# Kernel optimization log

Measured on AMD Instinct MI355X. Metric: run time of the kernel, lower is better.

Reference implementation:

```python
import jax, jax.numpy as jnp
import numpy as np

K_MASK = -2.3819763e+38
ROTARY_DIM = 80        # int(128 * 0.625), already even
ROPE_THETA = 1000000.0
NORM_EPS = 1e-6


def apply_rope(x, positions, head_dim, rope_theta):
    # x: [B, T, n, head_dim]; positions: [B, T]
    fraction = 2.0 * jnp.arange(0, head_dim // 2, dtype=jnp.float32) / head_dim
    timescale = rope_theta ** fraction                      # [hd/2]
    sinusoid = positions.astype(jnp.float32)[..., None] / timescale[None, None, :]
    sinusoid = sinusoid[..., None, :]                       # [B, T, 1, hd/2]
    sin = jnp.sin(sinusoid).astype(x.dtype)
    cos = jnp.cos(sinusoid).astype(x.dtype)
    first, second = jnp.split(x, 2, axis=-1)
    return jnp.concatenate(
        [first * cos - second * sin, second * cos + first * sin], axis=-1
    ).astype(x.dtype)


def rms_norm(x, w, eps=NORM_EPS):
    # Qwen3.5 convention: x/rms * (1 + w), w zero-initialized
    out = x * jax.lax.rsqrt(jnp.mean(x * x, axis=-1, keepdims=True) + eps)
    return out * (1.0 + w)


def setup_inputs() -> dict:
    B, T, D, N, K, H = 4, 1024, 4096, 32, 8, 128
    key = jax.random.key(0)
    ks = jax.random.split(key, 5)
    return {
        "x": jax.random.normal(ks[0], (B, T, D), jnp.float32),
        "positions": jnp.tile(jnp.arange(T, dtype=jnp.int32)[None, :], (B, 1)),
        "wq": jax.random.normal(ks[1], (D, N, 2 * H), jnp.float32) * 0.02,
        "wk": jax.random.normal(ks[2], (D, K, H), jnp.float32) * 0.02,
        "wv": jax.random.normal(ks[3], (D, K, H), jnp.float32) * 0.02,
        "wo": jax.random.normal(ks[4], (N, H, D), jnp.float32) * 0.02,
        "q_norm_w": jnp.zeros((H,), jnp.float32),
        "k_norm_w": jnp.zeros((H,), jnp.float32),
    }


def reference(x, positions, wq, wk, wv, wo, q_norm_w, k_norm_w):
    H = wk.shape[-1]
    # QKV projections; q_proj produces head_dim*2 -> (query, sigmoid gate)
    qg = jnp.einsum('BTD,DNH->BTNH', x, wq)            # [B,T,N,2H]
    q, gate = jnp.split(qg, 2, axis=-1)                # [B,T,N,H] each
    k = jnp.einsum('BSD,DKH->BSKH', x, wk)             # [B,S,K,H]
    v = jnp.einsum('BSD,DKH->BSKH', x, wv)             # [B,S,K,H]
    # per-head RMSNorm (Qwen3.5 style)
    q = rms_norm(q, q_norm_w)
    k = rms_norm(k, k_norm_w)
    # partial RoPE on first ROTARY_DIM dims of each head
    q = jnp.concatenate(
        [apply_rope(q[..., :ROTARY_DIM], positions, ROTARY_DIM, ROPE_THETA),
         q[..., ROTARY_DIM:]], axis=-1)
    k = jnp.concatenate(
        [apply_rope(k[..., :ROTARY_DIM], positions, ROTARY_DIM, ROPE_THETA),
         k[..., ROTARY_DIM:]], axis=-1)
    B, T, N, _ = q.shape
    Kh = k.shape[2]
    G = N // Kh                                        # GQA group size
    qg5 = q.reshape(B, T, Kh, G, H)
    scores = jnp.einsum('BTKGH,BSKH->BKGTS', qg5, k) * (H ** -0.5)
    causal = jnp.tril(jnp.ones((T, T), dtype=bool))    # [T,S]
    scores = jnp.where(causal[None, None, None, :, :], scores, K_MASK)
    probs = jax.nn.softmax(scores, axis=-1)
    out = jnp.einsum('BKGTS,BSKH->BTKGH', probs, v).reshape(B, T, N, H)
    out = out * jax.nn.sigmoid(gate)                   # gated attention output
    return jnp.einsum('BTNH,NHD->BTD', out, wo)
```

## Files before the change

### kernel.cpp

```cpp
#include <hip/hip_runtime.h>
#include <cstdint>
#include <cstddef>


typedef __attribute__((ext_vector_type(8))) short short8;
typedef __attribute__((ext_vector_type(4))) float float4v;

__device__ __forceinline__ unsigned short f2bf(float f) {
  unsigned u = __builtin_bit_cast(unsigned, f);
  u += 0x7fffu + ((u >> 16) & 1u);
  return (unsigned short)(u >> 16);
}
__device__ __forceinline__ float bf2f(unsigned short h) {
  unsigned u = ((unsigned)h) << 16;
  return __builtin_bit_cast(float, u);
}

__device__ __forceinline__ void gload_lds16(const void* g, void* l) {
  typedef const __attribute__((address_space(1))) void as1_cv;
  typedef __attribute__((address_space(3))) void as3_v;
  __builtin_amdgcn_global_load_lds((as1_cv*)g, (as3_v*)l, 16, 0, 0);
}

__global__ __launch_bounds__(256) void transpose_cvt(
    const float* __restrict__ src, unsigned short* __restrict__ dst,
    int R, int C) {
  __shared__ float tile[32][33];
  const int c0 = blockIdx.x * 32, r0 = blockIdx.y * 32;
  for (int i = threadIdx.y; i < 32; i += 8)
    tile[i][threadIdx.x] = src[(size_t)(r0 + i) * C + c0 + threadIdx.x];
  __syncthreads();
  for (int i = threadIdx.y; i < 32; i += 8)
    dst[(size_t)(c0 + i) * R + r0 + threadIdx.x] = f2bf(tile[threadIdx.x][i]);
}

__global__ __launch_bounds__(256) void cvt_f32_bf16(
    const float* __restrict__ src, unsigned short* __restrict__ dst, int n4) {
  int i = blockIdx.x * blockDim.x + threadIdx.x;
  if (i >= n4) return;
  float4 f = ((const float4*)src)[i];
  ushort4 o;
  o.x = f2bf(f.x); o.y = f2bf(f.y); o.z = f2bf(f.z); o.w = f2bf(f.w);
  ((ushort4*)dst)[i] = o;
}

__global__ __launch_bounds__(256) void v_transpose(
    const unsigned short* __restrict__ qkv, unsigned short* __restrict__ vtb) {
  __shared__ unsigned short tile[64][65];
  const int t0 = blockIdx.x * 64, h0 = blockIdx.y * 64;
  const int bk = blockIdx.z, b = bk >> 3, kh = bk & 7;
  const int tx = threadIdx.x & 63, ty = threadIdx.x >> 6;
  const unsigned short* src =
      qkv + (size_t)(b * 1024 + t0) * 10240 + 9216 + kh * 128 + h0;
  for (int i = ty; i < 64; i += 4)
    tile[i][tx] = src[(size_t)i * 10240 + tx];
  __syncthreads();
  unsigned short* dst = vtb + ((size_t)bk * 128 + h0) * 1024 + t0;
  for (int i = ty; i < 64; i += 4)
    dst[(size_t)i * 1024 + tx] = tile[tx][i];
}

template <bool BF16OUT>
__global__ __launch_bounds__(512, 2) void gemm_bt256(
    const unsigned short* __restrict__ A, const unsigned short* __restrict__ BT,
    void* __restrict__ Cv, int M, int N, int Kd) {
  __shared__ unsigned short As[4][256 * 32];
  __shared__ unsigned short Bs[4][256 * 32];

  const int tid = threadIdx.x;
  const int lane = tid & 63;
  const int wv = tid >> 6;
  const int wr = wv >> 2, wc = wv & 3;
  const int m0 = blockIdx.y * 256, n0 = blockIdx.x * 256;
  const int ml = lane & 15, q = lane >> 4;

  const int sr = tid >> 2;
  const int pc = tid & 3;
  const int gc = (pc ^ ((sr >> 1) & 3)) * 8;
  const unsigned short* gA0 = A + (size_t)(m0 + sr) * Kd + gc;
  const unsigned short* gB0 = BT + (size_t)(n0 + sr) * Kd + gc;
  const unsigned short* gA1 = gA0 + (size_t)128 * Kd;
  const unsigned short* gB1 = gB0 + (size_t)128 * Kd;
  const int lo0 = tid * 8;
  const int lo1 = 4096 + tid * 8;

  const int rdc = (q ^ ((ml >> 1) & 3)) * 8;
  const int aOff = (wr * 128 + ml) * 32 + rdc;
  const int bOff = (wc * 64 + ml) * 32 + rdc;

  float4v acc[8][4];
#pragma unroll
  for (int i = 0; i < 8; ++i)
#pragma unroll
    for (int j = 0; j < 4; ++j) acc[i][j] = (float4v)0.0f;

  const int NT = Kd >> 5;

#pragma unroll
  for (int t = 0; t < 3; ++t) {
    gload_lds16(gA0 + t * 32, &As[t][lo0]);
    gload_lds16(gA1 + t * 32, &As[t][lo1]);
    gload_lds16(gB0 + t * 32, &Bs[t][lo0]);
    gload_lds16(gB1 + t * 32, &Bs[t][lo1]);
  }
  asm volatile("s_waitcnt vmcnt(8)" ::: "memory");
  __builtin_amdgcn_s_barrier();

  for (int T = 0; T < NT; ++T) {
    const int buf = T & 3;
    const bool doStage = (T + 3 < NT);
    const int sb = (T + 3) & 3;
    const int gk = (T + 3) * 32;

    short8 bfr[4], af[4];
#pragma unroll
    for (int j = 0; j < 4; ++j)
      bfr[j] = *(const short8*)&Bs[buf][bOff + j * 512];
#pragma unroll
    for (int i = 0; i < 4; ++i)
      af[i] = *(const short8*)&As[buf][aOff + i * 512];
    if (doStage) {
      gload_lds16(gA0 + gk, &As[sb][lo0]);
      gload_lds16(gB0 + gk, &Bs[sb][lo0]);
    }
    __builtin_amdgcn_s_barrier();
    asm volatile("s_waitcnt lgkmcnt(0)" ::: "memory");
    __builtin_amdgcn_sched_barrier(0);
    __builtin_amdgcn_s_setprio(1);
#pragma unroll
    for (int i = 0; i < 4; ++i)
#pragma unroll
      for (int j = 0; j < 4; ++j)
        acc[i][j] = __builtin_amdgcn_mfma_f32_16x16x32_bf16(af[i], bfr[j], acc[i][j], 0, 0, 0);
    __builtin_amdgcn_s_setprio(0);
    __builtin_amdgcn_s_barrier();

#pragma unroll
    for (int i = 0; i < 4; ++i)
      af[i] = *(const short8*)&As[buf][aOff + 2048 + i * 512];
    if (doStage) {
      gload_lds16(gA1 + gk, &As[sb][lo1]);
      gload_lds16(gB1 + gk, &Bs[sb][lo1]);
    }
    __builtin_amdgcn_s_barrier();
    asm volatile("s_waitcnt lgkmcnt(0)" ::: "memory");
    __builtin_amdgcn_sched_barrier(0);
    __builtin_amdgcn_s_setprio(1);
#pragma unroll
    for (int i = 0; i < 4; ++i)
#pragma unroll
      for (int j = 0; j < 4; ++j)
        acc[4 + i][j] = __builtin_amdgcn_mfma_f32_16x16x32_bf16(af[i], bfr[j], acc[4 + i][j], 0, 0, 0);
    __builtin_amdgcn_s_setprio(0);
    if (T + 3 < NT)
      asm volatile("s_waitcnt vmcnt(8)" ::: "memory");
    else if (T + 2 < NT)
      asm volatile("s_waitcnt vmcnt(4)" ::: "memory");
    else if (T + 1 < NT)
      asm volatile("s_waitcnt vmcnt(0)" ::: "memory");
    __builtin_amdgcn_s_barrier();
  }

#pragma unroll
  for (int i = 0; i < 8; ++i) {
#pragma unroll
    for (int j = 0; j < 4; ++j) {
      const int grow = m0 + wr * 128 + i * 16 + q * 4;
      const int gcol = n0 + wc * 64 + j * 16 + ml;
#pragma unroll
      for (int r = 0; r < 4; ++r) {
        size_t idx = (size_t)(grow + r) * N + gcol;
        if constexpr (BF16OUT)
          ((unsigned short*)Cv)[idx] = f2bf(acc[i][j][r]);
        else
          ((float*)Cv)[idx] = acc[i][j][r];
      }
    }
  }
}

__global__ __launch_bounds__(256) void postproc_kernel(
    const unsigned short* __restrict__ qkv, const int* __restrict__ positions,
    const float* __restrict__ qnw, const float* __restrict__ knw,
    unsigned short* __restrict__ q_rot, unsigned short* __restrict__ sgb,
    unsigned short* __restrict__ k_rot) {
  const int wave = threadIdx.x >> 6, lane = threadIdx.x & 63;
  const int gslot = blockIdx.x * 4 + wave;
  const int m = gslot / 40, hs = gslot % 40;
  const int b = m >> 10, t = m & 1023;

  const unsigned short* base = (hs < 32)
      ? qkv + (size_t)m * 10240 + hs * 256
      : qkv + (size_t)m * 10240 + 8192 + (hs - 32) * 128;

  float v1 = bf2f(base[lane]);
  float v2 = bf2f(base[64 + lane]);

  float ss = v1 * v1 + v2 * v2;
  for (int off = 32; off > 0; off >>= 1) ss += __shfl_xor(ss, off);
  const float r = rsqrtf(ss * (1.0f / 128.0f) + 1e-6f);
  const float* nw = (hs < 32) ? qnw : knw;
  v1 *= r * (1.0f + nw[lane]);
  v2 *= r * (1.0f + nw[64 + lane]);

  const float pos = (float)positions[m];
  const int i1 = (lane < 40) ? lane : lane - 40;
  const float ang1 = pos * expf(-0.3453877639491068f * (float)i1);
  const float s1 = sinf(ang1), c1 = cosf(ang1);
  const float ang2 = pos * expf(-0.3453877639491068f * (float)(lane + 24));
  const float s2 = sinf(ang2), c2 = cosf(ang2);

  const float shA1 = __shfl(v1, (lane + 40) & 63);
  const float shA2 = __shfl(v2, (lane + 40) & 63);
  const float shX = __shfl(v1, (lane + 24) & 63);
  const float pA = (lane < 24) ? shA1 : shA2;
  const float o1 = (lane < 40) ? (v1 * c1 - pA * s1) : (v1 * c1 + shX * s1);
  const float o2 = (lane < 16) ? (v2 * c2 + shX * s2) : v2;

  if (hs < 32) {
    size_t qb = ((size_t)m * 32 + hs) * 128;
    q_rot[qb + lane] = f2bf(o1);
    q_rot[qb + 64 + lane] = f2bf(o2);
    float g1 = bf2f(base[128 + lane]), g2 = bf2f(base[192 + lane]);
    sgb[qb + lane] = f2bf(1.0f / (1.0f + expf(-g1)));
    sgb[qb + 64 + lane] = f2bf(1.0f / (1.0f + expf(-g2)));
  } else {
    const int kh = hs - 32;
    size_t kb = ((size_t)(b * 8 + kh) * 1024 + t) * 128;
    k_rot[kb + lane] = f2bf(o1);
    k_rot[kb + 64 + lane] = f2bf(o2);
  }
}

__global__ __launch_bounds__(256) void attn_kernel(
    const unsigned short* __restrict__ q_rot, const unsigned short* __restrict__ k_rot,
    const unsigned short* __restrict__ vt, const unsigned short* __restrict__ sgate,
    unsigned short* __restrict__ attn_out) {
  __shared__ unsigned short Ks[64 * 128];
  __shared__ unsigned short Vts[128 * 64];
  __shared__ unsigned short Ps[64 * 72];

  const int tid = threadIdx.x;
  const int lane = tid & 63, w = tid >> 6;
  const int qt = blockIdx.x & 15;
  const int n = (blockIdx.x >> 4) & 31;
  const int b = blockIdx.x >> 9;
  const int kh = n >> 2;
  const int t0 = qt * 64;
  const int ml = lane & 15, q = lane >> 4;
  const float SCALE = 0.08838834764831845f;

  short8 aq[4];
  {
    const unsigned short* qp =
        q_rot + (((size_t)(b * 1024 + t0 + w * 16 + ml)) * 32 + n) * 128 + q * 8;
#pragma unroll
    for (int ks = 0; ks < 4; ++ks) aq[ks] = *(const short8*)(qp + ks * 32);
  }

  float4v O[8];
#pragma unroll
  for (int i = 0; i < 8; ++i) O[i] = (float4v)0.0f;
  float mrow[4] = {-3e38f, -3e38f, -3e38f, -3e38f};
  float lrow[4] = {0.f, 0.f, 0.f, 0.f};

  const unsigned short* kbase = k_rot + (size_t)(b * 8 + kh) * 1024 * 128;
  const unsigned short* vbase = vt + (size_t)(b * 8 + kh) * 128 * 1024;
  const int rK = tid >> 4, cK = tid & 15;
  const int cKsw = (cK ^ rK) * 8;
  const int rV = tid >> 3, cV = tid & 7;
  const int cVsw = (cV ^ (rV & 7)) * 8;

  for (int si = 0; si <= qt; ++si) {
    const int s0 = si * 64;
#pragma unroll
    for (int it = 0; it < 4; ++it) {
      const int li = it * 256 + tid;
      gload_lds16(kbase + (size_t)(s0 + rK + it * 16) * 128 + cKsw, &Ks[li * 8]);
      gload_lds16(vbase + (size_t)(rV + it * 32) * 1024 + s0 + cVsw, &Vts[li * 8]);
    }
    __syncthreads();

    float4v Sv[4];
#pragma unroll
    for (int j = 0; j < 4; ++j) Sv[j] = (float4v)0.0f;
#pragma unroll
    for (int ks = 0; ks < 4; ++ks) {
#pragma unroll
      for (int j = 0; j < 4; ++j) {
        short8 bk = *(const short8*)&Ks[(j * 16 + ml) * 128 + (((ks * 4 + q) ^ ml) * 8)];
        Sv[j] = __builtin_amdgcn_mfma_f32_16x16x32_bf16(aq[ks], bk, Sv[j], 0, 0, 0);
      }
    }

    float P[4][4];
#pragma unroll
    for (int rr = 0; rr < 4; ++rr) {
      const int tg = t0 + w * 16 + q * 4 + rr;
      float vmax = -3e38f;
#pragma unroll
      for (int j = 0; j < 4; ++j) {
        const int sj = s0 + j * 16 + ml;
        float v = Sv[j][rr] * SCALE;
        if (sj > tg) v = -3.0e38f;
        P[j][rr] = v;
        vmax = fmaxf(vmax, v);
      }
      for (int off = 1; off < 16; off <<= 1) vmax = fmaxf(vmax, __shfl_xor(vmax, off));
      const float mnew = fmaxf(mrow[rr], vmax);
      const float alpha = __expf(mrow[rr] - mnew);
      mrow[rr] = mnew;
      lrow[rr] *= alpha;
#pragma unroll
      for (int ht = 0; ht < 8; ++ht) O[ht][rr] *= alpha;
      float rsum = 0.f;
#pragma unroll
      for (int j = 0; j < 4; ++j) {
        float e = __expf(P[j][rr] - mnew);
        P[j][rr] = e;
        rsum += e;
      }
      for (int off = 1; off < 16; off <<= 1) rsum += __shfl_xor(rsum, off);
      lrow[rr] += rsum;
    }

#pragma unroll
    for (int rr = 0; rr < 4; ++rr)
#pragma unroll
      for (int j = 0; j < 4; ++j)
        Ps[(w * 16 + q * 4 + rr) * 72 + j * 16 + ml] = f2bf(P[j][rr]);

#pragma unroll
    for (int ks = 0; ks < 2; ++ks) {
      short8 ap = *(const short8*)&Ps[(w * 16 + ml) * 72 + ks * 32 + q * 8];
#pragma unroll
      for (int ht = 0; ht < 8; ++ht) {
        short8 bv = *(const short8*)&Vts[(ht * 16 + ml) * 64 + (((ks * 4 + q) ^ (ml & 7)) * 8)];
        O[ht] = __builtin_amdgcn_mfma_f32_16x16x32_bf16(ap, bv, O[ht], 0, 0, 0);
      }
    }
    __syncthreads();
  }

#pragma unroll
  for (int rr = 0; rr < 4; ++rr) {
    const int tg = t0 + w * 16 + q * 4 + rr;
    const size_t ob = ((size_t)(b * 1024 + tg) * 32 + n) * 128;
    const float inv = 1.0f / lrow[rr];
#pragma unroll
    for (int ht = 0; ht < 8; ++ht) {
      const int h = ht * 16 + ml;
      attn_out[ob + h] = f2bf(O[ht][rr] * inv * bf2f(sgate[ob + h]));
    }
  }
}

extern "C" void kernel_launch(void* const* d_in, const int* in_sizes, int n_in,
                              void* d_out, int out_size, void* d_ws, size_t ws_size,
                              hipStream_t stream) {
  (void)in_sizes; (void)n_in; (void)out_size; (void)ws_size;
  const float* x = (const float*)d_in[0];
  const int* pos = (const int*)d_in[1];
  const float* wq = (const float*)d_in[2];
  const float* wk = (const float*)d_in[3];
  const float* wv = (const float*)d_in[4];
  const float* wo = (const float*)d_in[5];
  const float* qnw = (const float*)d_in[6];
  const float* knw = (const float*)d_in[7];
  float* out = (float*)d_out;

  unsigned short* ws = (unsigned short*)d_ws;
  unsigned short* x_bf = ws;
  unsigned short* wT = x_bf + 16777216;
  unsigned short* woT = wT + 41943040;
  unsigned short* qkv = woT + 16777216;
  unsigned short* q_rot = qkv + 41943040;
  unsigned short* sgb = q_rot + 16777216;
  unsigned short* k_rot = sgb + 16777216;
  unsigned short* vtb = k_rot + 4194304;
  unsigned short* attn = wT;

  dim3 tb(32, 8);
  transpose_cvt<<<dim3(256, 128), tb, 0, stream>>>(wq, wT, 4096, 8192);
  transpose_cvt<<<dim3(32, 128), tb, 0, stream>>>(wk, wT + (size_t)8192 * 4096, 4096, 1024);
  transpose_cvt<<<dim3(32, 128), tb, 0, stream>>>(wv, wT + (size_t)9216 * 4096, 4096, 1024);
  transpose_cvt<<<dim3(128, 128), tb, 0, stream>>>(wo, woT, 4096, 4096);
  cvt_f32_bf16<<<16384, 256, 0, stream>>>(x, x_bf, 4194304);

  gemm_bt256<true><<<dim3(40, 16), 512, 0, stream>>>(x_bf, wT, (void*)qkv, 4096, 10240, 4096);
  postproc_kernel<<<40960, 256, 0, stream>>>(qkv, pos, qnw, knw, q_rot, sgb, k_rot);
  v_transpose<<<dim3(16, 2, 32), 256, 0, stream>>>(qkv, vtb);
  attn_kernel<<<2048, 256, 0, stream>>>(q_rot, k_rot, vtb, sgb, attn);
  gemm_bt256<false><<<dim3(16, 16), 512, 0, stream>>>(attn, woT, (void*)out, 4096, 4096, 4096);
}
```

Before: 1.112 ms.

## Restructure GEMM mainloop to K=64 tiles with double buffering

Measured after the change: 1.093 ms. Within noise of the previous version (-1.7%).

```diff
diff --git a/kernel.cpp b/kernel.cpp
--- a/kernel.cpp
+++ b/kernel.cpp
@@ -64,8 +64,8 @@
 __global__ __launch_bounds__(512, 2) void gemm_bt256(
     const unsigned short* __restrict__ A, const unsigned short* __restrict__ BT,
     void* __restrict__ Cv, int M, int N, int Kd) {
-  __shared__ unsigned short As[4][256 * 32];
-  __shared__ unsigned short Bs[4][256 * 32];
+  __shared__ unsigned short As[2][16384];
+  __shared__ unsigned short Bs[2][16384];
 
   const int tid = threadIdx.x;
   const int lane = tid & 63;
@@ -74,19 +74,15 @@
   const int m0 = blockIdx.y * 256, n0 = blockIdx.x * 256;
   const int ml = lane & 15, q = lane >> 4;
 
-  const int sr = tid >> 2;
-  const int pc = tid & 3;
-  const int gc = (pc ^ ((sr >> 1) & 3)) * 8;
-  const unsigned short* gA0 = A + (size_t)(m0 + sr) * Kd + gc;
-  const unsigned short* gB0 = BT + (size_t)(n0 + sr) * Kd + gc;
-  const unsigned short* gA1 = gA0 + (size_t)128 * Kd;
-  const unsigned short* gB1 = gB0 + (size_t)128 * Kd;
-  const int lo0 = tid * 8;
-  const int lo1 = 4096 + tid * 8;
-
-  const int rdc = (q ^ ((ml >> 1) & 3)) * 8;
-  const int aOff = (wr * 128 + ml) * 32 + rdc;
-  const int bOff = (wc * 64 + ml) * 32 + rdc;
+  const int srow = tid >> 3;
+  const int sgc = ((tid & 7) ^ (srow & 7)) * 8;
+  const unsigned short* gA = A + (size_t)(m0 + srow) * Kd + sgc;
+  const unsigned short* gB = BT + (size_t)(n0 + srow) * Kd + sgc;
+  const int ldst = tid * 8;
+
+  const int rch = (q ^ (ml & 7)) * 8;
+  const int aBase = (wr * 128 + ml) * 64 + rch;
+  const int bBase = (wc * 64 + ml) * 64 + rch;
 
   float4v acc[8][4];
 #pragma unroll
@@ -94,69 +90,109 @@
 #pragma unroll
     for (int j = 0; j < 4; ++j) acc[i][j] = (float4v)0.0f;
 
-  const int NT = Kd >> 5;
-
-#pragma unroll
-  for (int t = 0; t < 3; ++t) {
-    gload_lds16(gA0 + t * 32, &As[t][lo0]);
-    gload_lds16(gA1 + t * 32, &As[t][lo1]);
-    gload_lds16(gB0 + t * 32, &Bs[t][lo0]);
-    gload_lds16(gB1 + t * 32, &Bs[t][lo1]);
-  }
-  asm volatile("s_waitcnt vmcnt(8)" ::: "memory");
+  const int NT = Kd >> 6;
+
+#pragma unroll
+  for (int h = 0; h < 4; ++h) {
+    const unsigned short* g = (h < 2) ? gA : gB;
+    const int hr = (h & 1) * 128;
+    unsigned short* l = (h < 2) ? &As[0][(h & 1) * 8192] : &Bs[0][(h & 1) * 8192];
+    gload_lds16(g + (size_t)hr * Kd, l + ldst);
+    gload_lds16(g + (size_t)(hr + 64) * Kd, l + ldst + 4096);
+  }
+  asm volatile("s_waitcnt vmcnt(0)" ::: "memory");
   __builtin_amdgcn_s_barrier();
 
+#pragma unroll 2
   for (int T = 0; T < NT; ++T) {
-    const int buf = T & 3;
-    const bool doStage = (T + 3 < NT);
-    const int sb = (T + 3) & 3;
-    const int gk = (T + 3) * 32;
-
-    short8 bfr[4], af[4];
-#pragma unroll
-    for (int j = 0; j < 4; ++j)
-      bfr[j] = *(const short8*)&Bs[buf][bOff + j * 512];
+    const unsigned short* Ab = As[T & 1];
+    const unsigned short* Bb = Bs[T & 1];
+    const bool doStage = (T + 1 < NT);
+
+    short8 af[8], ba[4], bb[4];
+#pragma unroll
+    for (int i = 0; i < 4; ++i) {
+      af[i * 2]     = *(const short8*)&Ab[aBase + i * 1024];
+      af[i * 2 + 1] = *(const short8*)&Ab[(aBase + i * 1024) ^ 32];
+    }
+#pragma unroll
+    for (int j = 0; j < 2; ++j) {
+      ba[j * 2]     = *(const short8*)&Bb[bBase + j * 1024];
+      ba[j * 2 + 1] = *(const short8*)&Bb[(bBase + j * 1024) ^ 32];
+    }
+    __builtin_amdgcn_sched_barrier(0);
+#pragma unroll
+    for (int j = 0; j < 2; ++j) {
+      bb[j * 2]     = *(const short8*)&Bb[bBase + 2048 + j * 1024];
+      bb[j * 2 + 1] = *(const short8*)&Bb[(bBase + 2048 + j * 1024) ^ 32];
+    }
+    asm volatile("s_waitcnt lgkmcnt(4)" ::: "memory");
+    __builtin_amdgcn_sched_barrier(0);
+    __builtin_amdgcn_s_setprio(1);
 #pragma unroll
     for (int i = 0; i < 4; ++i)
-      af[i] = *(const short8*)&As[buf][aOff + i * 512];
-    if (doStage) {
-      gload_lds16(gA0 + gk, &As[sb][lo0]);
-      gload_lds16(gB0 + gk, &Bs[sb][lo0]);
-    }
+#pragma unroll
+      for (int j = 0; j < 2; ++j) {
+        acc[i][j] = __builtin_amdgcn_mfma_f32_16x16x32_bf16(af[i * 2], ba[j * 2], acc[i][j], 0, 0, 0);
+        acc[i][j] = __builtin_amdgcn_mfma_f32_16x16x32_bf16(af[i * 2 + 1], ba[j * 2 + 1], acc[i][j], 0, 0, 0);
+      }
+    __builtin_amdgcn_s_setprio(0);
     __builtin_amdgcn_s_barrier();
+
     asm volatile("s_waitcnt lgkmcnt(0)" ::: "memory");
     __builtin_amdgcn_sched_barrier(0);
     __builtin_amdgcn_s_setprio(1);
 #pragma unroll
     for (int i = 0; i < 4; ++i)
 #pragma unroll
-      for (int j = 0; j < 4; ++j)
-        acc[i][j] = __builtin_amdgcn_mfma_f32_16x16x32_bf16(af[i], bfr[j], acc[i][j], 0, 0, 0);
+      for (int j = 0; j < 2; ++j) {
+        acc[i][2 + j] = __builtin_amdgcn_mfma_f32_16x16x32_bf16(af[i * 2], bb[j * 2], acc[i][2 + j], 0, 0, 0);
+        acc[i][2 + j] = __builtin_amdgcn_mfma_f32_16x16x32_bf16(af[i * 2 + 1], bb[j * 2 + 1], acc[i][2 + j], 0, 0, 0);
+      }
     __builtin_amdgcn_s_setprio(0);
     __builtin_amdgcn_s_barrier();
 
 #pragma unroll
-    for (int i = 0; i < 4; ++i)
-      af[i] = *(const short8*)&As[buf][aOff + 2048 + i * 512];
+    for (int i = 0; i < 4; ++i) {
+      af[i * 2]     = *(const short8*)&Ab[aBase + 4096 + i * 1024];
+      af[i * 2 + 1] = *(const short8*)&Ab[(aBase + 4096 + i * 1024) ^ 32];
+    }
+    __builtin_amdgcn_sched_barrier(0);
     if (doStage) {
-      gload_lds16(gA1 + gk, &As[sb][lo1]);
-      gload_lds16(gB1 + gk, &Bs[sb][lo1]);
-    }
-    __builtin_amdgcn_s_barrier();
+      const int sb = (T + 1) & 1;
+      const size_t kk = (size_t)(T + 1) * 64;
+#pragma unroll
+      for (int h = 0; h < 4; ++h) {
+        const unsigned short* g = (h < 2) ? gA : gB;
+        const int hr = (h & 1) * 128;
+        unsigned short* l = (h < 2) ? &As[sb][(h & 1) * 8192] : &Bs[sb][(h & 1) * 8192];
+        gload_lds16(g + (size_t)hr * Kd + kk, l + ldst);
+        gload_lds16(g + (size_t)(hr + 64) * Kd + kk, l + ldst + 4096);
+      }
+    }
     asm volatile("s_waitcnt lgkmcnt(0)" ::: "memory");
     __builtin_amdgcn_sched_barrier(0);
     __builtin_amdgcn_s_setprio(1);
 #pragma unroll
     for (int i = 0; i < 4; ++i)
 #pragma unroll
-      for (int j = 0; j < 4; ++j)
-        acc[4 + i][j] = __builtin_amdgcn_mfma_f32_16x16x32_bf16(af[i], bfr[j], acc[4 + i][j], 0, 0, 0);
+      for (int j = 0; j < 2; ++j) {
+        acc[4 + i][j] = __builtin_amdgcn_mfma_f32_16x16x32_bf16(af[i * 2], ba[j * 2], acc[4 + i][j], 0, 0, 0);
+        acc[4 + i][j] = __builtin_amdgcn_mfma_f32_16x16x32_bf16(af[i * 2 + 1], ba[j * 2 + 1], acc[4 + i][j], 0, 0, 0);
+      }
     __builtin_amdgcn_s_setprio(0);
-    if (T + 3 < NT)
-      asm volatile("s_waitcnt vmcnt(8)" ::: "memory");
-    else if (T + 2 < NT)
-      asm volatile("s_waitcnt vmcnt(4)" ::: "memory");
-    else if (T + 1 < NT)
+    __builtin_amdgcn_s_barrier();
+
+    __builtin_amdgcn_s_setprio(1);
+#pragma unroll
+    for (int i = 0; i < 4; ++i)
+#pragma unroll
+      for (int j = 0; j < 2; ++j) {
+        acc[4 + i][2 + j] = __builtin_amdgcn_mfma_f32_16x16x32_bf16(af[i * 2], bb[j * 2], acc[4 + i][2 + j], 0, 0, 0);
+        acc[4 + i][2 + j] = __builtin_amdgcn_mfma_f32_16x16x32_bf16(af[i * 2 + 1], bb[j * 2 + 1], acc[4 + i][2 + j], 0, 0, 0);
+      }
+    __builtin_amdgcn_s_setprio(0);
+    if (doStage)
       asm volatile("s_waitcnt vmcnt(0)" ::: "memory");
     __builtin_amdgcn_s_barrier();
   }
```
